# Kernel optimization log

Hardware: AMD Instinct MI355X
Metric: run time of the kernel (lower is better)

The kernel has to match this reference:

```python
import jax, jax.numpy as jnp
import numpy as np

EPS = 1e-10  # faithful to original: masked scores are set to eps, not -inf


def setup_inputs() -> dict:
    key = jax.random.key(0)
    ks = jax.random.split(key, 5)
    B, S, D, N, H = 2, 2048, 1024, 16, 64
    init_range = 0.02
    residual = jax.random.normal(ks[0], (B, S, D), dtype=jnp.float32)
    W_key = jax.random.normal(ks[1], (N, D, H), dtype=jnp.float32) * init_range
    W_query = jax.random.normal(ks[2], (N, D, H), dtype=jnp.float32) * init_range
    W_values = jax.random.normal(ks[3], (N, D, H), dtype=jnp.float32) * init_range
    W_output = jax.random.normal(ks[4], (N, H, D), dtype=jnp.float32) * init_range
    return {
        "residual": residual,
        "W_key": W_key, "W_query": W_query, "W_values": W_values, "W_output": W_output,
        "Bias_key": jnp.zeros((N, H), jnp.float32),
        "Bias_query": jnp.zeros((N, H), jnp.float32),
        "Bias_values": jnp.zeros((N, H), jnp.float32),
        "Bias_output": jnp.zeros((D,), jnp.float32),
    }


def reference(residual, W_key, W_query, W_values, W_output,
              Bias_key, Bias_query, Bias_values, Bias_output):
    B, S, D = residual.shape
    N, _, H = W_key.shape
    # projections: [b,s,n,h]
    keys = jnp.einsum('bse,neh->bsnh', residual, W_key) + Bias_key
    queries = jnp.einsum('bse,neh->bsnh', residual, W_query) + Bias_query
    values = jnp.einsum('bse,neh->bsnh', residual, W_values) + Bias_values
    # scores: [b,n,q,k]
    scores = jnp.einsum('bknh,bqnh->bnqk', keys, queries) / jnp.sqrt(jnp.asarray(H, scores_dtype(residual)))
    q_idx = jnp.arange(S)[:, None]
    k_idx = jnp.arange(S)[None, :]
    causal_mask = q_idx < k_idx  # future positions
    # QUIRK of original module: masked scores are assigned eps (~0), not -inf
    scores = jnp.where(causal_mask[None, None, :, :], jnp.asarray(EPS, scores.dtype), scores)
    probs = jax.nn.softmax(scores, axis=3)
    weighted = jnp.einsum('bnqk,bknh->bqnh', probs, values)
    out = jnp.einsum('bqnh,nhe->bqe', weighted, W_output) + Bias_output
    return out


def scores_dtype(x):
    return x.dtype
```

## Files before the change

### kernel.cpp

```cpp
#include <hip/hip_runtime.h>
#include <hip/hip_bf16.h>
#include <cmath>

typedef __bf16 bf16;
typedef __attribute__((ext_vector_type(8))) __bf16 bf16x8;
typedef __attribute__((ext_vector_type(4))) float f32x4;

#define B_ 2
#define S_ 2048
#define D_ 1024
#define N_ 16
#define H_ 64
#define LOG2E 1.44269504088896340736f

__device__ __forceinline__ void gload16(const bf16* g, bf16* l) {
  __builtin_amdgcn_global_load_lds(
      (const __attribute__((address_space(1))) void*)(g),
      (__attribute__((address_space(3))) void*)(l), 16, 0, 0);
}

__device__ __forceinline__ f32x4 mfma16(bf16x8 a, bf16x8 b, f32x4 c) {
  return __builtin_amdgcn_mfma_f32_16x16x32_bf16(a, b, c, 0, 0, 0);
}

__device__ __forceinline__ f32x4 zero4() {
  f32x4 v = {0.0f, 0.0f, 0.0f, 0.0f};
  return v;
}

__global__ __launch_bounds__(256) void cvt_kernel(
    const float* __restrict__ in, bf16* __restrict__ out, int n8) {
  int id = blockIdx.x * 256 + threadIdx.x;
  if (id >= n8) return;
  const float4* p = (const float4*)(in + (size_t)id * 8);
  float4 v0 = p[0], v1 = p[1];
  bf16x8 o;
  o[0] = (bf16)v0.x; o[1] = (bf16)v0.y; o[2] = (bf16)v0.z; o[3] = (bf16)v0.w;
  o[4] = (bf16)v1.x; o[5] = (bf16)v1.y; o[6] = (bf16)v1.z; o[7] = (bf16)v1.w;
  *(bf16x8*)(out + (size_t)id * 8) = o;
}

__global__ __launch_bounds__(256) void qkvw_transpose_kernel(
    const float* __restrict__ Wk, const float* __restrict__ Wq,
    const float* __restrict__ Wv, bf16* __restrict__ out) {
  __shared__ bf16 t[64][72];
  const int z = blockIdx.z;
  const float* W = (z < 16) ? Wk : (z < 32) ? Wq : Wv;
  const float* ing = W + (size_t)(z & 15) * (1024 * 64);
  bf16* outg = out + (size_t)z * (64 * 1024);
  const int r0 = blockIdx.x * 64;
  const int t8 = threadIdx.x & 7, trow = threadIdx.x >> 3;
#pragma unroll
  for (int p = 0; p < 2; ++p) {
    int r = trow + p * 32;
    const float4* src = (const float4*)(ing + (size_t)(r0 + r) * 64 + t8 * 8);
    float4 v0 = src[0], v1 = src[1];
    bf16x8 o;
    o[0] = (bf16)v0.x; o[1] = (bf16)v0.y; o[2] = (bf16)v0.z; o[3] = (bf16)v0.w;
    o[4] = (bf16)v1.x; o[5] = (bf16)v1.y; o[6] = (bf16)v1.z; o[7] = (bf16)v1.w;
    *(bf16x8*)(&t[r][t8 * 8]) = o;
  }
  __syncthreads();
#pragma unroll
  for (int p = 0; p < 2; ++p) {
    int c = trow + p * 32;
    bf16x8 v;
#pragma unroll
    for (int j = 0; j < 8; ++j) v[j] = t[t8 * 8 + j][c];
    *(bf16x8*)(outg + (size_t)c * 1024 + r0 + t8 * 8) = v;
  }
}

__global__ __launch_bounds__(256) void transpose_f32bf16_kernel(
    const float* __restrict__ in, bf16* __restrict__ out, int R, int C) {
  __shared__ bf16 t[64][72];
  const size_t mat = (size_t)R * C;
  const float* ing = in + (size_t)blockIdx.z * mat;
  bf16* outg = out + (size_t)blockIdx.z * mat;
  const int r0 = blockIdx.x * 64, c0 = blockIdx.y * 64;
  const int t8 = threadIdx.x & 7, trow = threadIdx.x >> 3;
#pragma unroll
  for (int p = 0; p < 2; ++p) {
    int r = trow + p * 32;
    const float4* src = (const float4*)(ing + (size_t)(r0 + r) * C + c0 + t8 * 8);
    float4 v0 = src[0], v1 = src[1];
    bf16x8 o;
    o[0] = (bf16)v0.x; o[1] = (bf16)v0.y; o[2] = (bf16)v0.z; o[3] = (bf16)v0.w;
    o[4] = (bf16)v1.x; o[5] = (bf16)v1.y; o[6] = (bf16)v1.z; o[7] = (bf16)v1.w;
    *(bf16x8*)(&t[r][t8 * 8]) = o;
  }
  __syncthreads();
#pragma unroll
  for (int p = 0; p < 2; ++p) {
    int c = trow + p * 32;
    bf16x8 v;
#pragma unroll
    for (int j = 0; j < 8; ++j) v[j] = t[t8 * 8 + j][c];
    *(bf16x8*)(outg + (size_t)(c0 + c) * R + r0 + t8 * 8) = v;
  }
}

__global__ __launch_bounds__(256) void transpose_bf16_kernel(
    const bf16* __restrict__ in, bf16* __restrict__ out, int R, int C) {
  __shared__ bf16 t[64][72];
  const size_t mat = (size_t)R * C;
  const bf16* ing = in + (size_t)blockIdx.z * mat;
  bf16* outg = out + (size_t)blockIdx.z * mat;
  const int r0 = blockIdx.x * 64, c0 = blockIdx.y * 64;
  const int t8 = threadIdx.x & 7, trow = threadIdx.x >> 3;
#pragma unroll
  for (int p = 0; p < 2; ++p) {
    int r = trow + p * 32;
    bf16x8 v = *(const bf16x8*)(ing + (size_t)(r0 + r) * C + c0 + t8 * 8);
    *(bf16x8*)(&t[r][t8 * 8]) = v;
  }
  __syncthreads();
#pragma unroll
  for (int p = 0; p < 2; ++p) {
    int c = trow + p * 32;
    bf16x8 v;
#pragma unroll
    for (int j = 0; j < 8; ++j) v[j] = t[t8 * 8 + j][c];
    *(bf16x8*)(outg + (size_t)(c0 + c) * R + r0 + t8 * 8) = v;
  }
}

__global__ __launch_bounds__(64) void sufv_tot_kernel(
    const bf16* __restrict__ Vp, float* __restrict__ tot) {
  const int hd = blockIdx.x, seg = blockIdx.y, h = threadIdx.x;
  const bf16* Vh = Vp + (size_t)hd * S_ * H_;
  float a = 0.0f;
  for (int k = seg * 128; k < seg * 128 + 128; ++k) a += (float)Vh[(size_t)k * H_ + h];
  tot[(hd * 16 + seg) * 64 + h] = a;
}

__global__ __launch_bounds__(64) void sufv_scan_kernel(
    const bf16* __restrict__ Vp, const float* __restrict__ tot,
    float* __restrict__ Suf) {
  const int hd = blockIdx.x, seg = blockIdx.y, h = threadIdx.x;
  const bf16* Vh = Vp + (size_t)hd * S_ * H_;
  float* Sh = Suf + (size_t)hd * S_ * H_;
  float a = 0.0f;
  for (int s2 = seg + 1; s2 < 16; ++s2) a += tot[(hd * 16 + s2) * 64 + h];
  for (int k = seg * 128 + 127; k >= seg * 128; --k) {
    Sh[(size_t)k * H_ + h] = a;
    a += (float)Vh[(size_t)k * H_ + h];
  }
}

__global__ __launch_bounds__(256) void gemm_proj_kernel(
    const bf16* __restrict__ A, const bf16* __restrict__ Wt_base,
    const float* __restrict__ bk, const float* __restrict__ bq,
    const float* __restrict__ bv, bf16* __restrict__ proj_base) {
  __shared__ bf16 As[128 * 64];
  __shared__ bf16 Bs[128 * 64];
  const int z = blockIdx.z;
  const bf16* Bt = Wt_base + (size_t)z * (1024 * 1024);
  const float* bias = (z == 0) ? bk : (z == 1 ? bq : bv);
  bf16* Out = proj_base + (size_t)z * ((size_t)B_ * N_ * S_ * H_);
  const int tid = threadIdx.x;
  const int w = tid >> 6, l = tid & 63, lan = l & 15, grp = l >> 4;
  const int mb = (w >> 1) * 64, nb = (w & 1) * 64;
  const int m0 = blockIdx.y * 128, n0 = blockIdx.x * 128;
  const int lrow8 = l >> 3;
  const int swl = ((l & 7) ^ lrow8) * 8;
  const int l7 = lan & 7;

  f32x4 acc[4][4];
#pragma unroll
  for (int i = 0; i < 4; ++i)
#pragma unroll
    for (int j = 0; j < 4; ++j) acc[i][j] = zero4();

  for (int kb = 0; kb < 1024; kb += 64) {
    __syncthreads();
#pragma unroll
    for (int i = 0; i < 4; ++i) {
      int ch = w * 4 + i;
      gload16(A + (size_t)(m0 + ch * 8 + lrow8) * 1024 + kb + swl, As + ch * 512);
      gload16(Bt + (size_t)(n0 + ch * 8 + lrow8) * 1024 + kb + swl, Bs + ch * 512);
    }
    __syncthreads();
#pragma unroll
    for (int kk = 0; kk < 2; ++kk) {
      bf16x8 a[4], b[4];
#pragma unroll
      for (int mf = 0; mf < 4; ++mf)
        a[mf] = *(const bf16x8*)(As + (mb + mf * 16 + lan) * 64 + (((grp + kk * 4) ^ l7) << 3));
#pragma unroll
      for (int nf = 0; nf < 4; ++nf)
        b[nf] = *(const bf16x8*)(Bs + (nb + nf * 16 + lan) * 64 + (((grp + kk * 4) ^ l7) << 3));
#pragma unroll
      for (int mf = 0; mf < 4; ++mf)
#pragma unroll
        for (int nf = 0; nf < 4; ++nf)
          acc[mf][nf] = mfma16(a[mf], b[nf], acc[mf][nf]);
    }
  }
#pragma unroll
  for (int nf = 0; nf < 4; ++nf) {
    int c = n0 + nb + nf * 16 + lan;
    float bs = bias[c];
    int n = c >> 6, h = c & 63;
#pragma unroll
    for (int mf = 0; mf < 4; ++mf) {
#pragma unroll
      for (int r = 0; r < 4; ++r) {
        int m = m0 + mb + mf * 16 + grp * 4 + r;
        int b = m >> 11, s = m & 2047;
        Out[((size_t)((b * N_ + n) * S_ + s)) * H_ + h] = (bf16)(acc[mf][nf][r] + bs);
      }
    }
  }
}

__global__ __launch_bounds__(256) void gemm_out_kernel(
    const bf16* __restrict__ A, const bf16* __restrict__ Bt,
    const float* __restrict__ bias, float* __restrict__ Out) {
  __shared__ bf16 As[128 * 64];
  __shared__ bf16 Bs[128 * 64];
  const int tid = threadIdx.x;
  const int w = tid >> 6, l = tid & 63, lan = l & 15, grp = l >> 4;
  const int mb = (w >> 1) * 64, nb = (w & 1) * 64;
  const int m0 = blockIdx.y * 128, n0 = blockIdx.x * 128;
  const int lrow8 = l >> 3;
  const int swl = ((l & 7) ^ lrow8) * 8;
  const int l7 = lan & 7;

  f32x4 acc[4][4];
#pragma unroll
  for (int i = 0; i < 4; ++i)
#pragma unroll
    for (int j = 0; j < 4; ++j) acc[i][j] = zero4();

  for (int kb = 0; kb < 1024; kb += 64) {
    __syncthreads();
#pragma unroll
    for (int i = 0; i < 4; ++i) {
      int ch = w * 4 + i;
      gload16(A + (size_t)(m0 + ch * 8 + lrow8) * 1024 + kb + swl, As + ch * 512);
      gload16(Bt + (size_t)(n0 + ch * 8 + lrow8) * 1024 + kb + swl, Bs + ch * 512);
    }
    __syncthreads();
#pragma unroll
    for (int kk = 0; kk < 2; ++kk) {
      bf16x8 a[4], b[4];
#pragma unroll
      for (int mf = 0; mf < 4; ++mf)
        a[mf] = *(const bf16x8*)(As + (mb + mf * 16 + lan) * 64 + (((grp + kk * 4) ^ l7) << 3));
#pragma unroll
      for (int nf = 0; nf < 4; ++nf)
        b[nf] = *(const bf16x8*)(Bs + (nb + nf * 16 + lan) * 64 + (((grp + kk * 4) ^ l7) << 3));
#pragma unroll
      for (int mf = 0; mf < 4; ++mf)
#pragma unroll
        for (int nf = 0; nf < 4; ++nf)
          acc[mf][nf] = mfma16(a[mf], b[nf], acc[mf][nf]);
    }
  }
#pragma unroll
  for (int nf = 0; nf < 4; ++nf) {
    int c = n0 + nb + nf * 16 + lan;
    float bs = bias[c];
#pragma unroll
    for (int mf = 0; mf < 4; ++mf) {
#pragma unroll
      for (int r = 0; r < 4; ++r) {
        int m = m0 + mb + mf * 16 + grp * 4 + r;
        Out[(size_t)m * 1024 + c] = acc[mf][nf][r] + bs;
      }
    }
  }
}

__global__ __launch_bounds__(256) void attn_kernel(
    const bf16* __restrict__ Qp, const bf16* __restrict__ Kp,
    const bf16* __restrict__ Vt, const float* __restrict__ Suf,
    bf16* __restrict__ Wtd) {
  __shared__ bf16 Ks[2][64 * 64];
  __shared__ bf16 Vs[2][64 * 64];
  __shared__ bf16 Ps[4][32 * 72];
  const int tid = threadIdx.x;
  const int w = tid >> 6, l = tid & 63, lan = l & 15, grp = l >> 4;
  const int bi = blockIdx.x;
  int x, hd;
  if (bi < 256) { x = 15 - (bi >> 5); hd = bi & 31; }
  else { int j = bi - 256; x = j >> 5; hd = j & 31; }
  const int ktiles = 2 * x + 2;
  const int qw = x * 128 + w * 32;
  const bf16* Qh = Qp + (size_t)hd * S_ * H_;
  const bf16* Kh = Kp + (size_t)hd * S_ * H_;
  const bf16* Vh = Vt + (size_t)hd * H_ * S_;
  const float* Sufh = Suf + (size_t)hd * S_ * H_;
  const int lrow8 = l >> 3;
  const int swl = ((l & 7) ^ lrow8) * 8;
  const int l7 = lan & 7;
  const float cexp = 0.125f * LOG2E;

#define STAGE(buf, kb_)                                                        \
  do {                                                                         \
    _Pragma("unroll") for (int i2 = 0; i2 < 2; ++i2) {                         \
      int ch = w * 2 + i2;                                                     \
      gload16(Kh + (size_t)((kb_) + ch * 8 + lrow8) * H_ + swl,                \
              &Ks[buf][ch * 512]);                                             \
      gload16(Vh + (size_t)(ch * 8 + lrow8) * S_ + (kb_) + swl,                \
              &Vs[buf][ch * 512]);                                             \
    }                                                                          \
  } while (0)

  bf16x8 qa[2][2];
#pragma unroll
  for (int qt = 0; qt < 2; ++qt)
#pragma unroll
    for (int kf = 0; kf < 2; ++kf)
      qa[qt][kf] = *(const bf16x8*)(Qh + (size_t)(qw + qt * 16 + lan) * H_ + grp * 8 + kf * 32);

  f32x4 o[2][4];
  float psum[2] = {0.0f, 0.0f};
#pragma unroll
  for (int qt = 0; qt < 2; ++qt)
#pragma unroll
    for (int hf = 0; hf < 4; ++hf) o[qt][hf] = zero4();

  bf16* Pw = &Ps[w][0];

  STAGE(0, 0);
  for (int tt = 0; tt < ktiles; ++tt) {
    const int kb = tt * 64;
    const int cur = tt & 1;
    if (tt + 1 < ktiles) {
      STAGE(cur ^ 1, kb + 64);
      asm volatile("s_waitcnt vmcnt(4)" ::: "memory");
    } else {
      asm volatile("s_waitcnt vmcnt(0)" ::: "memory");
    }
    __builtin_amdgcn_s_barrier();

    if (kb <= qw + 31) {
      const bf16* Kc = &Ks[cur][0];
      const bf16* Vc = &Vs[cur][0];

      f32x4 s2[4][2];
#pragma unroll
      for (int k2 = 0; k2 < 4; ++k2)
#pragma unroll
        for (int qt = 0; qt < 2; ++qt) s2[k2][qt] = zero4();
      __builtin_amdgcn_s_setprio(1);
#pragma unroll
      for (int kf = 0; kf < 2; ++kf) {
        bf16x8 kfr[4];
#pragma unroll
        for (int k2 = 0; k2 < 4; ++k2)
          kfr[k2] = *(const bf16x8*)(Kc + (k2 * 16 + lan) * 64 + (((grp + kf * 4) ^ l7) << 3));
#pragma unroll
        for (int k2 = 0; k2 < 4; ++k2)
#pragma unroll
          for (int qt = 0; qt < 2; ++qt)
            s2[k2][qt] = mfma16(kfr[k2], qa[qt][kf], s2[k2][qt]);
      }
      __builtin_amdgcn_s_setprio(0);

      const bool maskt = (kb + 63 > qw);
#pragma unroll
      for (int qt = 0; qt < 2; ++qt) {
        const int q_g = qw + qt * 16 + lan;
#pragma unroll
        for (int k2 = 0; k2 < 4; ++k2) {
          f32x4 p;
#pragma unroll
          for (int r = 0; r < 4; ++r) p[r] = exp2f(s2[k2][qt][r] * cexp);
          if (maskt) {
            const int kg0 = kb + k2 * 16 + grp * 4;
#pragma unroll
            for (int r = 0; r < 4; ++r)
              if (kg0 + r > q_g) p[r] = 0.0f;
          }
          psum[qt] += (p[0] + p[1]) + (p[2] + p[3]);
          unsigned plo, phi;
          asm("v_cvt_pk_bf16_f32 %0, %1, %2" : "=v"(plo) : "v"(p[0]), "v"(p[1]));
          asm("v_cvt_pk_bf16_f32 %0, %1, %2" : "=v"(phi) : "v"(p[2]), "v"(p[3]));
          uint2 u; u.x = plo; u.y = phi;
          *(uint2*)(Pw + (qt * 16 + lan) * 72 + k2 * 16 + grp * 4) = u;
        }
      }

      __builtin_amdgcn_s_setprio(1);
#pragma unroll
      for (int ks = 0; ks < 2; ++ks) {
        bf16x8 pa[2], vb[4];
#pragma unroll
        for (int qt = 0; qt < 2; ++qt)
          pa[qt] = *(const bf16x8*)(Pw + (qt * 16 + lan) * 72 + grp * 8 + ks * 32);
#pragma unroll
        for (int hf = 0; hf < 4; ++hf)
          vb[hf] = *(const bf16x8*)(Vc + (hf * 16 + lan) * 64 + (((grp + ks * 4) ^ l7) << 3));
#pragma unroll
        for (int qt = 0; qt < 2; ++qt)
#pragma unroll
          for (int hf = 0; hf < 4; ++hf)
            o[qt][hf] = mfma16(pa[qt], vb[hf], o[qt][hf]);
      }
      __builtin_amdgcn_s_setprio(0);
    }
    __builtin_amdgcn_s_barrier();
  }
#undef STAGE

#pragma unroll
  for (int qt = 0; qt < 2; ++qt) {
    psum[qt] += __shfl_xor(psum[qt], 16);
    psum[qt] += __shfl_xor(psum[qt], 32);
  }

  const size_t outbase = (size_t)(hd >> 4) * S_ * (N_ * H_) + (size_t)(hd & 15) * H_;
#pragma unroll
  for (int qt = 0; qt < 2; ++qt) {
#pragma unroll
    for (int r = 0; r < 4; ++r) {
      const int q_g = qw + qt * 16 + grp * 4 + r;
      const float ps = __shfl(psum[qt], grp * 4 + r);
      const float inv = 1.0f / (ps + (float)(2047 - q_g));
#pragma unroll
      for (int hf = 0; hf < 4; ++hf) {
        const int h = hf * 16 + lan;
        const float suf = Sufh[(size_t)q_g * H_ + h];
        Wtd[outbase + (size_t)q_g * (N_ * H_) + h] = (bf16)((o[qt][hf][r] + suf) * inv);
      }
    }
  }
}

extern "C" void kernel_launch(void* const* d_in, const int* in_sizes, int n_in,
                              void* d_out, int out_size, void* d_ws, size_t ws_size,
                              hipStream_t stream) {
  const float* residual = (const float*)d_in[0];
  const float* Wk = (const float*)d_in[1];
  const float* Wq = (const float*)d_in[2];
  const float* Wv = (const float*)d_in[3];
  const float* Wo = (const float*)d_in[4];
  const float* Bk = (const float*)d_in[5];
  const float* Bq = (const float*)d_in[6];
  const float* Bv = (const float*)d_in[7];
  const float* Bo = (const float*)d_in[8];
  float* outp = (float*)d_out;

  char* ws = (char*)d_ws;
  const size_t MB = 1024 * 1024;
  bf16* Abf = (bf16*)(ws + 0 * MB);
  bf16* Wot = (bf16*)(ws + 8 * MB);
  bf16* Wkt = (bf16*)(ws + 10 * MB);
  bf16* Kp  = (bf16*)(ws + 16 * MB);
  bf16* Qp  = (bf16*)(ws + 24 * MB);
  bf16* Vp  = (bf16*)(ws + 32 * MB);
  bf16* Vtp = (bf16*)(ws + 40 * MB);
  float* tot = (float*)(ws + 48 * MB);
  bf16* Wtd = Abf;
  float* Suf = (float*)d_out;
  (void)in_sizes; (void)n_in; (void)out_size; (void)ws_size;

  cvt_kernel<<<2048, 256, 0, stream>>>(residual, Abf, (B_ * S_ * D_) / 8);

  qkvw_transpose_kernel<<<dim3(16, 1, 48), 256, 0, stream>>>(Wk, Wq, Wv, Wkt);
  transpose_f32bf16_kernel<<<dim3(16, 16, 1), 256, 0, stream>>>(Wo, Wot, 1024, 1024);

  gemm_proj_kernel<<<dim3(8, 32, 3), 256, 0, stream>>>(Abf, Wkt, Bk, Bq, Bv, Kp);

  sufv_tot_kernel<<<dim3(32, 16), 64, 0, stream>>>(Vp, tot);
  sufv_scan_kernel<<<dim3(32, 16), 64, 0, stream>>>(Vp, tot, Suf);

  transpose_bf16_kernel<<<dim3(32, 1, 32), 256, 0, stream>>>(Vp, Vtp, 2048, 64);

  attn_kernel<<<512, 256, 0, stream>>>(Qp, Kp, Vtp, Suf, Wtd);

  gemm_out_kernel<<<dim3(8, 32, 1), 256, 0, stream>>>(Wtd, Wot, Bo, outp);

  (void)Qp;
}
```

Measured before the change: 164.4 us.

## Load K/V fragments directly from global into registers and widen suffix-sum parallelism

The attention kernel drops the LDS-staged, double-buffered K/V tiles and their block barriers. Each wave now loads its K fragments straight from global memory into registers, ping-ponging two register sets, and reads V fragments directly per tile. Each wave also runs only the key tiles it needs rather than the block-wide count. Separately, the V suffix-sum kernels use 64 segments instead of 16, with a 4-way split reduction in the total kernel, to expose more parallelism. The cost is higher register pressure and redundant global/L2 traffic, since each of the 4 waves fetches the same K/V without sharing through LDS.

```diff
diff --git a/kernel.cpp b/kernel.cpp
--- a/kernel.cpp
+++ b/kernel.cpp
@@ -125,13 +125,20 @@
   }
 }
 
-__global__ __launch_bounds__(64) void sufv_tot_kernel(
+__global__ __launch_bounds__(256) void sufv_tot_kernel(
     const bf16* __restrict__ Vp, float* __restrict__ tot) {
-  const int hd = blockIdx.x, seg = blockIdx.y, h = threadIdx.x;
+  __shared__ float red[4][64];
+  const int hd = blockIdx.x, seg = blockIdx.y;
+  const int h = threadIdx.x & 63, sub = threadIdx.x >> 6;
   const bf16* Vh = Vp + (size_t)hd * S_ * H_;
   float a = 0.0f;
-  for (int k = seg * 128; k < seg * 128 + 128; ++k) a += (float)Vh[(size_t)k * H_ + h];
-  tot[(hd * 16 + seg) * 64 + h] = a;
+  const int k0 = seg * 32 + sub * 8;
+#pragma unroll
+  for (int k = 0; k < 8; ++k) a += (float)Vh[(size_t)(k0 + k) * H_ + h];
+  red[sub][h] = a;
+  __syncthreads();
+  if (sub == 0)
+    tot[(hd * 64 + seg) * 64 + h] = red[0][h] + red[1][h] + red[2][h] + red[3][h];
 }
 
 __global__ __launch_bounds__(64) void sufv_scan_kernel(
@@ -141,8 +148,8 @@
   const bf16* Vh = Vp + (size_t)hd * S_ * H_;
   float* Sh = Suf + (size_t)hd * S_ * H_;
   float a = 0.0f;
-  for (int s2 = seg + 1; s2 < 16; ++s2) a += tot[(hd * 16 + s2) * 64 + h];
-  for (int k = seg * 128 + 127; k >= seg * 128; --k) {
+  for (int s2 = seg + 1; s2 < 64; ++s2) a += tot[(hd * 64 + s2) * 64 + h];
+  for (int k = seg * 32 + 31; k >= seg * 32; --k) {
     Sh[(size_t)k * H_ + h] = a;
     a += (float)Vh[(size_t)k * H_ + h];
   }
@@ -277,8 +284,6 @@
     const bf16* __restrict__ Qp, const bf16* __restrict__ Kp,
     const bf16* __restrict__ Vt, const float* __restrict__ Suf,
     bf16* __restrict__ Wtd) {
-  __shared__ bf16 Ks[2][64 * 64];
-  __shared__ bf16 Vs[2][64 * 64];
   __shared__ bf16 Ps[4][32 * 72];
   const int tid = threadIdx.x;
   const int w = tid >> 6, l = tid & 63, lan = l & 15, grp = l >> 4;
@@ -286,27 +291,13 @@
   int x, hd;
   if (bi < 256) { x = 15 - (bi >> 5); hd = bi & 31; }
   else { int j = bi - 256; x = j >> 5; hd = j & 31; }
-  const int ktiles = 2 * x + 2;
   const int qw = x * 128 + w * 32;
   const bf16* Qh = Qp + (size_t)hd * S_ * H_;
   const bf16* Kh = Kp + (size_t)hd * S_ * H_;
   const bf16* Vh = Vt + (size_t)hd * H_ * S_;
   const float* Sufh = Suf + (size_t)hd * S_ * H_;
-  const int lrow8 = l >> 3;
-  const int swl = ((l & 7) ^ lrow8) * 8;
-  const int l7 = lan & 7;
   const float cexp = 0.125f * LOG2E;
-
-#define STAGE(buf, kb_)                                                        \
-  do {                                                                         \
-    _Pragma("unroll") for (int i2 = 0; i2 < 2; ++i2) {                         \
-      int ch = w * 2 + i2;                                                     \
-      gload16(Kh + (size_t)((kb_) + ch * 8 + lrow8) * H_ + swl,                \
-              &Ks[buf][ch * 512]);                                             \
-      gload16(Vh + (size_t)(ch * 8 + lrow8) * S_ + (kb_) + swl,                \
-              &Vs[buf][ch * 512]);                                             \
-    }                                                                          \
-  } while (0)
+  bf16* Pw = &Ps[w][0];
 
   bf16x8 qa[2][2];
 #pragma unroll
@@ -322,89 +313,75 @@
 #pragma unroll
     for (int hf = 0; hf < 4; ++hf) o[qt][hf] = zero4();
 
-  bf16* Pw = &Ps[w][0];
-
-  STAGE(0, 0);
-  for (int tt = 0; tt < ktiles; ++tt) {
-    const int kb = tt * 64;
-    const int cur = tt & 1;
-    if (tt + 1 < ktiles) {
-      STAGE(cur ^ 1, kb + 64);
-      asm volatile("s_waitcnt vmcnt(4)" ::: "memory");
-    } else {
-      asm volatile("s_waitcnt vmcnt(0)" ::: "memory");
-    }
-    __builtin_amdgcn_s_barrier();
-
-    if (kb <= qw + 31) {
-      const bf16* Kc = &Ks[cur][0];
-      const bf16* Vc = &Vs[cur][0];
-
-      f32x4 s2[4][2];
-#pragma unroll
-      for (int k2 = 0; k2 < 4; ++k2)
-#pragma unroll
-        for (int qt = 0; qt < 2; ++qt) s2[k2][qt] = zero4();
-      __builtin_amdgcn_s_setprio(1);
-#pragma unroll
-      for (int kf = 0; kf < 2; ++kf) {
-        bf16x8 kfr[4];
-#pragma unroll
-        for (int k2 = 0; k2 < 4; ++k2)
-          kfr[k2] = *(const bf16x8*)(Kc + (k2 * 16 + lan) * 64 + (((grp + kf * 4) ^ l7) << 3));
-#pragma unroll
-        for (int k2 = 0; k2 < 4; ++k2)
-#pragma unroll
-          for (int qt = 0; qt < 2; ++qt)
-            s2[k2][qt] = mfma16(kfr[k2], qa[qt][kf], s2[k2][qt]);
-      }
-      __builtin_amdgcn_s_setprio(0);
-
-      const bool maskt = (kb + 63 > qw);
-#pragma unroll
-      for (int qt = 0; qt < 2; ++qt) {
-        const int q_g = qw + qt * 16 + lan;
-#pragma unroll
-        for (int k2 = 0; k2 < 4; ++k2) {
-          f32x4 p;
-#pragma unroll
-          for (int r = 0; r < 4; ++r) p[r] = exp2f(s2[k2][qt][r] * cexp);
-          if (maskt) {
-            const int kg0 = kb + k2 * 16 + grp * 4;
-#pragma unroll
-            for (int r = 0; r < 4; ++r)
-              if (kg0 + r > q_g) p[r] = 0.0f;
-          }
-          psum[qt] += (p[0] + p[1]) + (p[2] + p[3]);
-          unsigned plo, phi;
-          asm("v_cvt_pk_bf16_f32 %0, %1, %2" : "=v"(plo) : "v"(p[0]), "v"(p[1]));
-          asm("v_cvt_pk_bf16_f32 %0, %1, %2" : "=v"(phi) : "v"(p[2]), "v"(p[3]));
-          uint2 u; u.x = plo; u.y = phi;
-          *(uint2*)(Pw + (qt * 16 + lan) * 72 + k2 * 16 + grp * 4) = u;
-        }
-      }
-
-      __builtin_amdgcn_s_setprio(1);
-#pragma unroll
-      for (int ks = 0; ks < 2; ++ks) {
-        bf16x8 pa[2], vb[4];
-#pragma unroll
-        for (int qt = 0; qt < 2; ++qt)
-          pa[qt] = *(const bf16x8*)(Pw + (qt * 16 + lan) * 72 + grp * 8 + ks * 32);
-#pragma unroll
-        for (int hf = 0; hf < 4; ++hf)
-          vb[hf] = *(const bf16x8*)(Vc + (hf * 16 + lan) * 64 + (((grp + ks * 4) ^ l7) << 3));
-#pragma unroll
-        for (int qt = 0; qt < 2; ++qt)
-#pragma unroll
-          for (int hf = 0; hf < 4; ++hf)
-            o[qt][hf] = mfma16(pa[qt], vb[hf], o[qt][hf]);
-      }
-      __builtin_amdgcn_s_setprio(0);
-    }
-    __builtin_amdgcn_s_barrier();
-  }
-#undef STAGE
+#define LOADK(SET, kb_)                                                        \
+  do {                                                                         \
+    _Pragma("unroll") for (int k2 = 0; k2 < 4; ++k2)                           \
+      _Pragma("unroll") for (int kf = 0; kf < 2; ++kf)                         \
+        SET[k2][kf] = *(const bf16x8*)(Kh + (size_t)((kb_) + k2 * 16 + lan) * H_ + grp * 8 + kf * 32); \
+  } while (0)
+
+#define COMPUTE(SET, kb_)                                                      \
+  do {                                                                         \
+    const int kb = (kb_);                                                      \
+    bf16x8 vb[4][2];                                                           \
+    _Pragma("unroll") for (int hf = 0; hf < 4; ++hf)                           \
+      _Pragma("unroll") for (int ks = 0; ks < 2; ++ks)                         \
+        vb[hf][ks] = *(const bf16x8*)(Vh + (size_t)(hf * 16 + lan) * S_ + kb + grp * 8 + ks * 32); \
+    f32x4 s2[4][2];                                                            \
+    _Pragma("unroll") for (int k2 = 0; k2 < 4; ++k2)                           \
+      _Pragma("unroll") for (int qt = 0; qt < 2; ++qt) s2[k2][qt] = zero4();   \
+    __builtin_amdgcn_s_setprio(1);                                             \
+    _Pragma("unroll") for (int kf = 0; kf < 2; ++kf)                           \
+      _Pragma("unroll") for (int k2 = 0; k2 < 4; ++k2)                         \
+        _Pragma("unroll") for (int qt = 0; qt < 2; ++qt)                       \
+          s2[k2][qt] = mfma16(SET[k2][kf], qa[qt][kf], s2[k2][qt]);            \
+    __builtin_amdgcn_s_setprio(0);                                             \
+    const bool maskt = (kb + 63 > qw);                                         \
+    _Pragma("unroll") for (int qt = 0; qt < 2; ++qt) {                         \
+      const int q_g = qw + qt * 16 + lan;                                      \
+      _Pragma("unroll") for (int k2 = 0; k2 < 4; ++k2) {                       \
+        f32x4 p;                                                               \
+        _Pragma("unroll") for (int r = 0; r < 4; ++r)                          \
+          p[r] = exp2f(s2[k2][qt][r] * cexp);                                  \
+        if (maskt) {                                                           \
+          const int kg0 = kb + k2 * 16 + grp * 4;                              \
+          _Pragma("unroll") for (int r = 0; r < 4; ++r)                        \
+            if (kg0 + r > q_g) p[r] = 0.0f;                                    \
+        }                                                                      \
+        psum[qt] += (p[0] + p[1]) + (p[2] + p[3]);                             \
+        unsigned plo, phi;                                                     \
+        asm("v_cvt_pk_bf16_f32 %0, %1, %2" : "=v"(plo) : "v"(p[0]), "v"(p[1]));\
+        asm("v_cvt_pk_bf16_f32 %0, %1, %2" : "=v"(phi) : "v"(p[2]), "v"(p[3]));\
+        uint2 u; u.x = plo; u.y = phi;                                         \
+        *(uint2*)(Pw + (qt * 16 + lan) * 72 + k2 * 16 + grp * 4) = u;          \
+      }                                                                        \
+    }                                                                          \
+    __builtin_amdgcn_s_setprio(1);                                             \
+    _Pragma("unroll") for (int ks = 0; ks < 2; ++ks) {                         \
+      bf16x8 pa[2];                                                            \
+      _Pragma("unroll") for (int qt = 0; qt < 2; ++qt)                         \
+        pa[qt] = *(const bf16x8*)(Pw + (qt * 16 + lan) * 72 + grp * 8 + ks * 32); \
+      _Pragma("unroll") for (int qt = 0; qt < 2; ++qt)                         \
+        _Pragma("unroll") for (int hf = 0; hf < 4; ++hf)                       \
+          o[qt][hf] = mfma16(pa[qt], vb[hf][ks], o[qt][hf]);                   \
+    }                                                                          \
+    __builtin_amdgcn_s_setprio(0);                                             \
+  } while (0)
+
+  const int nt = ((qw + 31) >> 6) + 1;
+  bf16x8 kfrA[4][2], kfrB[4][2];
+  LOADK(kfrA, 0);
+  int t = 0;
+  for (;;) {
+    if (t + 1 < nt) LOADK(kfrB, (t + 1) * 64);
+    COMPUTE(kfrA, t * 64);
+    if (++t >= nt) break;
+    if (t + 1 < nt) LOADK(kfrA, (t + 1) * 64);
+    COMPUTE(kfrB, t * 64);
+    if (++t >= nt) break;
+  }
+#undef LOADK
+#undef COMPUTE
 
 #pragma unroll
   for (int qt = 0; qt < 2; ++qt) {
@@ -465,8 +442,8 @@
 
   gemm_proj_kernel<<<dim3(8, 32, 3), 256, 0, stream>>>(Abf, Wkt, Bk, Bq, Bv, Kp);
 
-  sufv_tot_kernel<<<dim3(32, 16), 64, 0, stream>>>(Vp, tot);
-  sufv_scan_kernel<<<dim3(32, 16), 64, 0, stream>>>(Vp, tot, Suf);
+  sufv_tot_kernel<<<dim3(32, 64), 256, 0, stream>>>(Vp, tot);
+  sufv_scan_kernel<<<dim3(32, 64), 64, 0, stream>>>(Vp, tot, Suf);
 
   transpose_bf16_kernel<<<dim3(32, 1, 32), 256, 0, stream>>>(Vp, Vtp, 2048, 64);
 
```

Result: slower. 187.0 us (+13.8%).

## Split long causal attention rows across two blocks and combine partial results

Applied to the files above, without the earlier changes.

Attention blocks covering the 8 longest query groups are split into two halves along the key range. Each half writes unnormalized partial outputs and row sums to scratch, and a new combine kernel adds the halves with the suffix-sum term and normalizes. This gives 768 blocks instead of 512 and evens out the per-block work. The suffix-sum scan is also refined to 64 segments with a 4-way in-block reduction and stores bf16 in place over V, which halves suffix traffic at the cost of bf16 rounding of suffix sums.

```diff
diff --git a/kernel.cpp b/kernel.cpp
--- a/kernel.cpp
+++ b/kernel.cpp
@@ -3,6 +3,7 @@
 #include <cmath>
 
 typedef __bf16 bf16;
+typedef __attribute__((ext_vector_type(4))) __bf16 bf16x4;
 typedef __attribute__((ext_vector_type(8))) __bf16 bf16x8;
 typedef __attribute__((ext_vector_type(4))) float f32x4;
 
@@ -125,26 +126,32 @@
   }
 }
 
-__global__ __launch_bounds__(64) void sufv_tot_kernel(
+__global__ __launch_bounds__(256) void sufv_tot_kernel(
     const bf16* __restrict__ Vp, float* __restrict__ tot) {
-  const int hd = blockIdx.x, seg = blockIdx.y, h = threadIdx.x;
+  __shared__ float red[4][64];
+  const int hd = blockIdx.x, seg = blockIdx.y;
+  const int h = threadIdx.x & 63, sub = threadIdx.x >> 6;
   const bf16* Vh = Vp + (size_t)hd * S_ * H_;
   float a = 0.0f;
-  for (int k = seg * 128; k < seg * 128 + 128; ++k) a += (float)Vh[(size_t)k * H_ + h];
-  tot[(hd * 16 + seg) * 64 + h] = a;
+  const int k0 = seg * 32 + sub * 8;
+#pragma unroll
+  for (int k = 0; k < 8; ++k) a += (float)Vh[(size_t)(k0 + k) * H_ + h];
+  red[sub][h] = a;
+  __syncthreads();
+  if (sub == 0)
+    tot[(hd * 64 + seg) * 64 + h] = red[0][h] + red[1][h] + red[2][h] + red[3][h];
 }
 
 __global__ __launch_bounds__(64) void sufv_scan_kernel(
-    const bf16* __restrict__ Vp, const float* __restrict__ tot,
-    float* __restrict__ Suf) {
+    bf16* __restrict__ VS, const float* __restrict__ tot) {
   const int hd = blockIdx.x, seg = blockIdx.y, h = threadIdx.x;
-  const bf16* Vh = Vp + (size_t)hd * S_ * H_;
-  float* Sh = Suf + (size_t)hd * S_ * H_;
+  bf16* Vh = VS + (size_t)hd * S_ * H_;
   float a = 0.0f;
-  for (int s2 = seg + 1; s2 < 16; ++s2) a += tot[(hd * 16 + s2) * 64 + h];
-  for (int k = seg * 128 + 127; k >= seg * 128; --k) {
-    Sh[(size_t)k * H_ + h] = a;
-    a += (float)Vh[(size_t)k * H_ + h];
+  for (int s2 = seg + 1; s2 < 64; ++s2) a += tot[(hd * 64 + s2) * 64 + h];
+  for (int k = seg * 32 + 31; k >= seg * 32; --k) {
+    const float v = (float)Vh[(size_t)k * H_ + h];
+    Vh[(size_t)k * H_ + h] = (bf16)a;
+    a += v;
   }
 }
 
@@ -275,23 +282,27 @@
 
 __global__ __launch_bounds__(256) void attn_kernel(
     const bf16* __restrict__ Qp, const bf16* __restrict__ Kp,
-    const bf16* __restrict__ Vt, const float* __restrict__ Suf,
-    bf16* __restrict__ Wtd) {
+    const bf16* __restrict__ Vt, const bf16* __restrict__ Suf,
+    bf16* __restrict__ Wtd, float* __restrict__ PoA, float* __restrict__ PoB,
+    float* __restrict__ PpA, float* __restrict__ PpB) {
   __shared__ bf16 Ks[2][64 * 64];
   __shared__ bf16 Vs[2][64 * 64];
   __shared__ bf16 Ps[4][32 * 72];
   const int tid = threadIdx.x;
   const int w = tid >> 6, l = tid & 63, lan = l & 15, grp = l >> 4;
   const int bi = blockIdx.x;
-  int x, hd;
-  if (bi < 256) { x = 15 - (bi >> 5); hd = bi & 31; }
-  else { int j = bi - 256; x = j >> 5; hd = j & 31; }
-  const int ktiles = 2 * x + 2;
+  const int qq = bi >> 8;
+  const int j = bi & 255;
+  const int hd = j & 31, wv = j >> 5;
+  int x, t0, t1;
+  if (qq == 0)      { x = 15 - wv; t0 = 0;     t1 = x + 1; }
+  else if (qq == 1) { x = 15 - wv; t0 = x + 1; t1 = 2 * x + 2; }
+  else              { x = wv;      t0 = 0;     t1 = 2 * x + 2; }
   const int qw = x * 128 + w * 32;
   const bf16* Qh = Qp + (size_t)hd * S_ * H_;
   const bf16* Kh = Kp + (size_t)hd * S_ * H_;
   const bf16* Vh = Vt + (size_t)hd * H_ * S_;
-  const float* Sufh = Suf + (size_t)hd * S_ * H_;
+  const bf16* Sufh = Suf + (size_t)hd * S_ * H_;
   const int lrow8 = l >> 3;
   const int swl = ((l & 7) ^ lrow8) * 8;
   const int l7 = lan & 7;
@@ -324,11 +335,11 @@
 
   bf16* Pw = &Ps[w][0];
 
-  STAGE(0, 0);
-  for (int tt = 0; tt < ktiles; ++tt) {
+  STAGE(0, t0 * 64);
+  for (int tt = t0; tt < t1; ++tt) {
     const int kb = tt * 64;
-    const int cur = tt & 1;
-    if (tt + 1 < ktiles) {
+    const int cur = (tt - t0) & 1;
+    if (tt + 1 < t1) {
       STAGE(cur ^ 1, kb + 64);
       asm volatile("s_waitcnt vmcnt(4)" ::: "memory");
     } else {
@@ -412,21 +423,66 @@
     psum[qt] += __shfl_xor(psum[qt], 32);
   }
 
+  if (qq == 2) {
+    const size_t outbase = (size_t)(hd >> 4) * S_ * (N_ * H_) + (size_t)(hd & 15) * H_;
+#pragma unroll
+    for (int qt = 0; qt < 2; ++qt) {
+#pragma unroll
+      for (int r = 0; r < 4; ++r) {
+        const int q_g = qw + qt * 16 + grp * 4 + r;
+        const float ps = __shfl(psum[qt], grp * 4 + r);
+        const float inv = 1.0f / (ps + (float)(2047 - q_g));
+#pragma unroll
+        for (int hf = 0; hf < 4; ++hf) {
+          const int h = hf * 16 + lan;
+          const float suf = (float)Sufh[(size_t)q_g * H_ + h];
+          Wtd[outbase + (size_t)q_g * (N_ * H_) + h] = (bf16)((o[qt][hf][r] + suf) * inv);
+        }
+      }
+    }
+  } else {
+    float* Po = (qq == 0) ? PoA : PoB;
+    float* Pp = (qq == 0) ? PpA : PpB;
+    const int pb = (hd * 8 + (x - 8)) * 128 + w * 32;
+#pragma unroll
+    for (int qt = 0; qt < 2; ++qt) {
+#pragma unroll
+      for (int r = 0; r < 4; ++r) {
+        const int rl = qt * 16 + grp * 4 + r;
+        const float ps = __shfl(psum[qt], grp * 4 + r);
+        if (lan == 0) Pp[pb + rl] = ps;
+#pragma unroll
+        for (int hf = 0; hf < 4; ++hf)
+          Po[(size_t)(pb + rl) * 64 + hf * 16 + lan] = o[qt][hf][r];
+      }
+    }
+  }
+}
+
+__global__ __launch_bounds__(256) void combine_kernel(
+    const float* __restrict__ PoA, const float* __restrict__ PoB,
+    const float* __restrict__ PpA, const float* __restrict__ PpB,
+    const bf16* __restrict__ Suf, bf16* __restrict__ Wtd) {
+  const int hd = blockIdx.x >> 3, xi = blockIdx.x & 7;
+  const int x = xi + 8;
+  const int pb = (hd * 8 + xi) * 128;
   const size_t outbase = (size_t)(hd >> 4) * S_ * (N_ * H_) + (size_t)(hd & 15) * H_;
 #pragma unroll
-  for (int qt = 0; qt < 2; ++qt) {
-#pragma unroll
-    for (int r = 0; r < 4; ++r) {
-      const int q_g = qw + qt * 16 + grp * 4 + r;
-      const float ps = __shfl(psum[qt], grp * 4 + r);
-      const float inv = 1.0f / (ps + (float)(2047 - q_g));
-#pragma unroll
-      for (int hf = 0; hf < 4; ++hf) {
-        const int h = hf * 16 + lan;
-        const float suf = Sufh[(size_t)q_g * H_ + h];
-        Wtd[outbase + (size_t)q_g * (N_ * H_) + h] = (bf16)((o[qt][hf][r] + suf) * inv);
-      }
-    }
+  for (int it = 0; it < 8; ++it) {
+    const int e = it * 256 + threadIdx.x;
+    const int rl = e >> 4, h4 = (e & 15) * 4;
+    const int q_g = x * 128 + rl;
+    const float Z = PpA[pb + rl] + PpB[pb + rl] + (float)(2047 - q_g);
+    const float inv = 1.0f / Z;
+    const float4 a = *(const float4*)(PoA + (size_t)(pb + rl) * 64 + h4);
+    const float4 b = *(const float4*)(PoB + (size_t)(pb + rl) * 64 + h4);
+    const bf16x4 s4 = *(const bf16x4*)(Suf + ((size_t)hd * S_ + q_g) * 64 + h4);
+    bf16x4 ov;
+    ov[0] = (bf16)((a.x + b.x + (float)s4[0]) * inv);
+    ov[1] = (bf16)((a.y + b.y + (float)s4[1]) * inv);
+    ov[2] = (bf16)((a.z + b.z + (float)s4[2]) * inv);
+    ov[3] = (bf16)((a.w + b.w + (float)s4[3]) * inv);
+    *(bf16x4*)(Wtd + outbase + (size_t)q_g * (N_ * H_) + h4) = ov;
   }
 }
 
@@ -453,9 +509,13 @@
   bf16* Qp  = (bf16*)(ws + 24 * MB);
   bf16* Vp  = (bf16*)(ws + 32 * MB);
   bf16* Vtp = (bf16*)(ws + 40 * MB);
-  float* tot = (float*)(ws + 48 * MB);
   bf16* Wtd = Abf;
-  float* Suf = (float*)d_out;
+  float* PpA = (float*)(ws + 10 * MB);
+  float* PpB = (float*)(ws + 10 * MB + 128 * 1024);
+  float* tot = (float*)(ws + 10 * MB + 256 * 1024);
+  bf16* Suf = Vp;
+  float* PoA = (float*)d_out;
+  float* PoB = (float*)d_out + 2 * 1024 * 1024;
   (void)in_sizes; (void)n_in; (void)out_size; (void)ws_size;
 
   cvt_kernel<<<2048, 256, 0, stream>>>(residual, Abf, (B_ * S_ * D_) / 8);
@@ -465,14 +525,13 @@
 
   gemm_proj_kernel<<<dim3(8, 32, 3), 256, 0, stream>>>(Abf, Wkt, Bk, Bq, Bv, Kp);
 
-  sufv_tot_kernel<<<dim3(32, 16), 64, 0, stream>>>(Vp, tot);
-  sufv_scan_kernel<<<dim3(32, 16), 64, 0, stream>>>(Vp, tot, Suf);
-
+  sufv_tot_kernel<<<dim3(32, 64), 256, 0, stream>>>(Vp, tot);
   transpose_bf16_kernel<<<dim3(32, 1, 32), 256, 0, stream>>>(Vp, Vtp, 2048, 64);
-
-  attn_kernel<<<512, 256, 0, stream>>>(Qp, Kp, Vtp, Suf, Wtd);
+  sufv_scan_kernel<<<dim3(32, 64), 64, 0, stream>>>(Vp, tot);
+
+  attn_kernel<<<768, 256, 0, stream>>>(Qp, Kp, Vtp, Suf, Wtd, PoA, PoB, PpA, PpB);
+
+  combine_kernel<<<256, 256, 0, stream>>>(PoA, PoB, PpA, PpB, Suf, Wtd);
 
   gemm_out_kernel<<<dim3(8, 32, 1), 256, 0, stream>>>(Wtd, Wot, Bo, outp);
-
-  (void)Qp;
-}
+}
```

New measurement: 158.6 us. 3.5% less time.
